# Kernel optimization log

Hardware: AMD Instinct MI355X
Metric: run time of the kernel (lower is better)

The kernel has to match this reference:

```python
import jax, jax.numpy as jnp
import numpy as np

DIM = 1024
NUM_HEADS = 16
HEAD_DIM = DIM // NUM_HEADS


def setup_inputs() -> dict:
    key = jax.random.key(0)
    k1, k2, k3, k4 = jax.random.split(key, 4)
    x = jax.random.normal(k1, (4, 4096, DIM), dtype=jnp.float32)
    # nn.Linear(dim, 3*dim, bias=False): weight [3*dim, dim]
    w_qkv = jax.random.normal(k2, (3 * DIM, DIM), dtype=jnp.float32) * (1.0 / np.sqrt(DIM))
    # nn.Linear(dim, dim): weight [dim, dim], bias [dim]
    w_proj = jax.random.normal(k3, (DIM, DIM), dtype=jnp.float32) * (1.0 / np.sqrt(DIM))
    b_proj = jax.random.normal(k4, (DIM,), dtype=jnp.float32) * 0.01
    return {"x": x, "w_qkv": w_qkv, "w_proj": w_proj, "b_proj": b_proj}


def reference(x, w_qkv, w_proj, b_proj):
    B, N, C = x.shape
    H, D = NUM_HEADS, C // NUM_HEADS
    # qkv projection: [B,N,3C] -> [3,B,H,N,D]
    qkv = (x @ w_qkv.T).reshape(B, N, 3, H, D).transpose(2, 0, 3, 1, 4)
    q, k, v = qkv[0], qkv[1], qkv[2]
    # elu(x)+1 feature map
    q = jax.nn.elu(q) + 1.0
    k = jax.nn.elu(k) + 1.0
    # kv outer-product aggregation: [B,H,D,D]
    kv = jnp.einsum('bhnd,bhne->bhde', k, v)
    # numerator: [B,H,N,D]
    num = jnp.einsum('bhnd,bhde->bhne', q, kv)
    # normalizer: [B,H,N]
    z = 1.0 / (jnp.einsum('bhnd,bhd->bhn', q, k.sum(axis=2)) + 1e-6)
    out = num * z[..., None]  # [B,H,N,D]
    out = out.transpose(0, 2, 1, 3).reshape(B, N, C)
    return out @ w_proj.T + b_proj
```

## Files before the change

kernel.cpp:

```cpp
#include <hip/hip_runtime.h>
#include <hip/hip_bf16.h>
#include <stdint.h>


typedef unsigned short u16;
typedef __attribute__((ext_vector_type(4))) float f32x4;
typedef __attribute__((ext_vector_type(8))) __bf16 bf16x8;
typedef __attribute__((ext_vector_type(4))) unsigned short us4;
typedef __attribute__((ext_vector_type(8))) unsigned short us8;

typedef __attribute__((address_space(3))) unsigned as3u;
typedef const __attribute__((address_space(1))) unsigned as1u;

__device__ __forceinline__ float bf2f(u16 u) {
  union { unsigned i; float f; } x; x.i = ((unsigned)u) << 16; return x.f;
}
__device__ __forceinline__ u16 f2bf(float f) {
  union { float f; unsigned i; } x; x.f = f;
  return (u16)((x.i + 0x7FFFu + ((x.i >> 16) & 1u)) >> 16);
}
__device__ __forceinline__ void gload16(const u16* g, u16* l) {
  __builtin_amdgcn_global_load_lds((as1u*)g, (as3u*)l, 16, 0, 0);
}
__device__ __forceinline__ bf16x8 ld8(const u16* p) { return *(const bf16x8*)p; }

#define BAR asm volatile("s_barrier" ::: "memory")
#define VMC4 asm volatile("s_waitcnt vmcnt(4)" ::: "memory")
#define VMC0 asm volatile("s_waitcnt vmcnt(0)" ::: "memory")

__global__ __launch_bounds__(256) void cvt_kernel(const float* __restrict__ src,
                                                  u16* __restrict__ dst, int n4) {
  int i = blockIdx.x * 256 + threadIdx.x;
  if (i < n4) {
    f32x4 v = ((const f32x4*)src)[i];
    us4 o;
    o[0] = f2bf(v[0]); o[1] = f2bf(v[1]); o[2] = f2bf(v[2]); o[3] = f2bf(v[3]);
    ((us4*)dst)[i] = o;
  }
}

template <int EPI>
__global__ __launch_bounds__(512) void gemm256(
    const u16* __restrict__ A, const u16* __restrict__ B, int Ncols,
    u16* __restrict__ oQ, u16* __restrict__ oKT, u16* __restrict__ oVT,
    const float* __restrict__ bias, float* __restrict__ oF) {
  constexpr int K = 1024;
  constexpr int NITER = 8;
  __shared__ u16 lds[2][2][256 * 64];

  const int nTn = Ncols >> 8;
  const int nwg = gridDim.x;
  const int bid = blockIdx.x;
  const int swz = (bid & 7) * (nwg >> 3) + (bid >> 3);
  const int tm = swz / nTn, tn = swz % nTn;
  const int m0 = tm << 8, n0 = tn << 8;
  const int t = threadIdx.x;
  const int w = t >> 6, lane = t & 63;
  const int wm = w >> 2, wn = w & 3;
  const int l15 = lane & 15, l4 = lane >> 4;

  const u16* Ab = A + (size_t)m0 * K;
  const u16* Bb = B + (size_t)n0 * K;

  int srcoff[2][2];
  #pragma unroll
  for (int l = 0; l < 2; ++l) {
    int c = l * 512 + t;
    int row = c >> 3, ch = c & 7;
    #pragma unroll
    for (int h = 0; h < 2; ++h) {
      int r = row + h * 128;
      srcoff[l][h] = r * K + (ch ^ (r & 7)) * 8;
    }
  }

#define STAGE(mat, buf, h, kt)                                                \
  {                                                                           \
    const u16* gsrc = ((mat) ? Bb : Ab) + (kt) * 64;                          \
    _Pragma("unroll") for (int l = 0; l < 2; ++l)                             \
        gload16(gsrc + srcoff[l][h],                                          \
                &lds[buf][mat][(l * 512 + w * 64) * 8 + (h) * 128 * 64]);     \
  }

#define LDA(buf, q)                                                           \
  _Pragma("unroll") for (int i = 0; i < 2; ++i)                               \
  _Pragma("unroll") for (int kk = 0; kk < 2; ++kk) {                          \
    int row = wm * 128 + (q) * 32 + i * 16 + l15;                             \
    int ch = (kk * 4 + l4) ^ (row & 7);                                       \
    a[i][kk] = ld8(&lds[buf][0][row * 64 + ch * 8]);                          \
  }

#define LDB(buf)                                                              \
  _Pragma("unroll") for (int j = 0; j < 4; ++j)                               \
  _Pragma("unroll") for (int kk = 0; kk < 2; ++kk) {                          \
    int row = wn * 64 + j * 16 + l15;                                         \
    int ch = (kk * 4 + l4) ^ (row & 7);                                       \
    b[j][kk] = ld8(&lds[buf][1][row * 64 + ch * 8]);                          \
  }

#define MFMA16(q)                                                             \
  __builtin_amdgcn_s_setprio(1);                                              \
  _Pragma("unroll") for (int i = 0; i < 2; ++i)                               \
  _Pragma("unroll") for (int kk = 0; kk < 2; ++kk)                            \
  _Pragma("unroll") for (int j = 0; j < 4; ++j)                               \
    acc[(q) * 2 + i][j] = __builtin_amdgcn_mfma_f32_16x16x32_bf16(            \
        a[i][kk], b[j][kk], acc[(q) * 2 + i][j], 0, 0, 0);                    \
  __builtin_amdgcn_s_setprio(0);

  f32x4 acc[8][4] = {};
  bf16x8 a[2][2], b[4][2];

  STAGE(1, 0, 0, 0); STAGE(1, 0, 1, 0);
  STAGE(0, 0, 0, 0); STAGE(0, 0, 1, 0);
  STAGE(1, 1, 0, 1); STAGE(1, 1, 1, 1);
  VMC4;
  BAR;

  for (int J = 0; J < NITER; ++J) {
    const int t2 = 2 * J + 2, t3 = 2 * J + 3;
    const bool more = (J < NITER - 1);
    LDB(0); LDA(0, 0);
    STAGE(0, 1, 0, 2 * J + 1);
    BAR; MFMA16(0); BAR;
    LDA(0, 1);
    STAGE(0, 1, 1, 2 * J + 1);
    BAR; MFMA16(1); BAR;
    LDA(0, 2);
    if (more) STAGE(1, 0, 0, t2);
    BAR; MFMA16(2); BAR;
    LDA(0, 3);
    if (more) STAGE(1, 0, 1, t2);
    BAR; MFMA16(3);
    if (more) { VMC4; } else { VMC0; }
    BAR;
    LDB(1); LDA(1, 0);
    if (more) STAGE(0, 0, 0, t2);
    BAR; MFMA16(0); BAR;
    LDA(1, 1);
    if (more) STAGE(0, 0, 1, t2);
    BAR; MFMA16(1); BAR;
    LDA(1, 2);
    if (more) STAGE(1, 1, 0, t3);
    BAR; MFMA16(2); BAR;
    LDA(1, 3);
    if (more) STAGE(1, 1, 1, t3);
    BAR; MFMA16(3);
    if (more) { VMC4; } else { VMC0; }
    BAR;
  }

  if constexpr (EPI == 0) {
    #pragma unroll
    for (int j = 0; j < 4; ++j) {
      const int col = n0 + wn * 64 + j * 16 + l15;
      const int part = col >> 10, cc = col & 1023;
      const int h = cc >> 6, d = cc & 63;
      #pragma unroll
      for (int fi = 0; fi < 8; ++fi) {
        const int mbase = m0 + wm * 128 + fi * 16 + l4 * 4;
        const int bb = mbase >> 12, n = mbase & 4095;
        const int bh = bb * 16 + h;
        if (part == 0) {
          #pragma unroll
          for (int r = 0; r < 4; ++r) {
            float val = acc[fi][j][r];
            val = val > 0.f ? val + 1.f : __expf(val);
            oQ[(((size_t)bh) * 4096 + n + r) * 64 + d] = f2bf(val);
          }
        } else {
          us4 o;
          #pragma unroll
          for (int r = 0; r < 4; ++r) {
            float val = acc[fi][j][r];
            if (part == 1) val = val > 0.f ? val + 1.f : __expf(val);
            o[r] = f2bf(val);
          }
          u16* dst = (part == 1) ? oKT : oVT;
          *(us4*)&dst[(((size_t)bh) * 64 + d) * 4096 + n] = o;
        }
      }
    }
  } else {
    #pragma unroll
    for (int fi = 0; fi < 8; ++fi) {
      const int mbase = m0 + wm * 128 + fi * 16 + l4 * 4;
      #pragma unroll
      for (int j = 0; j < 4; ++j) {
        const int col = n0 + wn * 64 + j * 16 + l15;
        #pragma unroll
        for (int r = 0; r < 4; ++r)
          oF[(size_t)(mbase + r) * 1024 + col] = acc[fi][j][r] + bias[col];
      }
    }
  }
#undef STAGE
#undef LDA
#undef LDB
#undef MFMA16
}

__global__ __launch_bounds__(256) void kv_mfma(const u16* __restrict__ kTg,
                                               const u16* __restrict__ vTg,
                                               float* __restrict__ kv_part,
                                               float* __restrict__ ksum_part) {
  __shared__ u16 kTl[64 * 256];
  __shared__ u16 vTl[64 * 256];
  const int blk = blockIdx.x;
  const int bh = blk >> 4, s = blk & 15;
  const int n0 = s * 256;
  const int t = threadIdx.x;
  const int w = t >> 6, lane = t & 63;
  const int wr = w >> 1, wc = w & 1;
  const int l15 = lane & 15, l4 = lane >> 4;

  const u16* kg = kTg + ((size_t)bh * 64) * 4096 + n0;
  const u16* vg = vTg + ((size_t)bh * 64) * 4096 + n0;
  #pragma unroll
  for (int i = 0; i < 8; ++i) {
    int c = i * 256 + t;
    int row = c >> 5, ch = c & 31;
    int sch = (ch & ~7) | ((ch ^ row) & 7);
    gload16(kg + (size_t)row * 4096 + sch * 8, &kTl[(i * 256 + w * 64) * 8]);
    gload16(vg + (size_t)row * 4096 + sch * 8, &vTl[(i * 256 + w * 64) * 8]);
  }
  __syncthreads();

  {
    const int row = t >> 2, q4 = t & 3;
    float sum = 0.f;
    #pragma unroll
    for (int j = 0; j < 8; ++j) {
      int p = q4 * 8 + ((j + row) & 7);
      us8 u = *(const us8*)&kTl[row * 256 + p * 8];
      #pragma unroll
      for (int x = 0; x < 8; ++x) sum += bf2f(u[x]);
    }
    sum += __shfl_xor(sum, 1);
    sum += __shfl_xor(sum, 2);
    if ((t & 3) == 0) ksum_part[((size_t)s * 64 + bh) * 64 + row] = sum;
  }

  f32x4 acc[2][2] = {};
  #pragma unroll
  for (int kk = 0; kk < 8; ++kk) {
    bf16x8 a[2], b[2];
    #pragma unroll
    for (int i = 0; i < 2; ++i) {
      int row = wr * 32 + i * 16 + l15;
      int p = (kk * 4 + l4) ^ (row & 7);
      a[i] = ld8(&kTl[row * 256 + p * 8]);
    }
    #pragma unroll
    for (int j = 0; j < 2; ++j) {
      int row = wc * 32 + j * 16 + l15;
      int p = (kk * 4 + l4) ^ (row & 7);
      b[j] = ld8(&vTl[row * 256 + p * 8]);
    }
    #pragma unroll
    for (int i = 0; i < 2; ++i)
      #pragma unroll
      for (int j = 0; j < 2; ++j)
        acc[i][j] = __builtin_amdgcn_mfma_f32_16x16x32_bf16(a[i], b[j], acc[i][j], 0, 0, 0);
  }
  float* dst = kv_part + ((size_t)s * 64 + bh) * 4096;
  #pragma unroll
  for (int i = 0; i < 2; ++i)
    #pragma unroll
    for (int j = 0; j < 2; ++j)
      #pragma unroll
      for (int r = 0; r < 4; ++r) {
        int d = wr * 32 + i * 16 + l4 * 4 + r;
        int e = wc * 32 + j * 16 + l15;
        dst[e * 64 + d] = acc[i][j][r];
      }
}

__global__ __launch_bounds__(256) void cvt_kv(const float* __restrict__ kv_part,
                                              const float* __restrict__ ksum_part,
                                              u16* __restrict__ kvTb) {
  const int bh = blockIdx.x;
  const int t = threadIdx.x;
  #pragma unroll
  for (int i = 0; i < 20; ++i) {
    int idx = i * 256 + t;
    int row = idx >> 6, d = idx & 63;
    float s = 0.f;
    if (row < 64) {
      #pragma unroll
      for (int p = 0; p < 16; ++p)
        s += kv_part[((size_t)p * 64 + bh) * 4096 + idx];
    } else if (row == 64) {
      #pragma unroll
      for (int p = 0; p < 16; ++p)
        s += ksum_part[((size_t)p * 64 + bh) * 64 + d];
    }
    kvTb[(size_t)bh * 5120 + idx] = f2bf(s);
  }
}

__global__ __launch_bounds__(256) void numz_mfma(const u16* __restrict__ qg,
                                                 const u16* __restrict__ kvTb,
                                                 u16* __restrict__ attn) {
  __shared__ u16 ql[128 * 64];
  __shared__ u16 bl[80 * 64];
  const int blk = blockIdx.x;
  const int bh = blk >> 5, c5 = blk & 31;
  const int t = threadIdx.x;
  const int w = t >> 6, lane = t & 63;
  const int l15 = lane & 15, l4 = lane >> 4;
  const int bb = bh >> 4, h = bh & 15;

  const u16* qp = qg + ((size_t)bh * 4096 + c5 * 128) * 64;
  #pragma unroll
  for (int i = 0; i < 4; ++i) {
    int c = i * 256 + t;
    int row = c >> 3, ch = c & 7;
    gload16(qp + (size_t)row * 64 + ((ch ^ row) & 7) * 8, &ql[(i * 256 + w * 64) * 8]);
  }
  {
    const us4* bsrc = (const us4*)(kvTb + (size_t)bh * 5120);
    #pragma unroll
    for (int i = 0; i < 5; ++i) {
      int idx = i * 256 + t;
      int row = idx >> 4;
      ((us4*)bl)[idx ^ ((row & 7) << 1)] = bsrc[idx];
    }
  }
  __syncthreads();

  f32x4 acc[2][5] = {};
  #pragma unroll
  for (int kk = 0; kk < 2; ++kk) {
    bf16x8 a[2], b[5];
    #pragma unroll
    for (int i = 0; i < 2; ++i) {
      int row = w * 32 + i * 16 + l15;
      int p = (kk * 4 + l4) ^ (row & 7);
      a[i] = ld8(&ql[row * 64 + p * 8]);
    }
    #pragma unroll
    for (int j = 0; j < 5; ++j) {
      int row = j * 16 + l15;
      int p = (kk * 4 + l4) ^ (row & 7);
      b[j] = ld8(&bl[row * 64 + p * 8]);
    }
    #pragma unroll
    for (int i = 0; i < 2; ++i)
      #pragma unroll
      for (int j = 0; j < 5; ++j)
        acc[i][j] = __builtin_amdgcn_mfma_f32_16x16x32_bf16(a[i], b[j], acc[i][j], 0, 0, 0);
  }

  #pragma unroll
  for (int i = 0; i < 2; ++i)
    #pragma unroll
    for (int r = 0; r < 4; ++r) {
      int m = w * 32 + i * 16 + l4 * 4 + r;
      int n = c5 * 128 + m;
      float zv = __shfl(acc[i][4][r], lane & 48);
      float zz = 1.f / (zv + 1e-6f);
      u16* op = attn + ((size_t)bb * 4096 + n) * 1024 + h * 64;
      #pragma unroll
      for (int j = 0; j < 4; ++j)
        op[j * 16 + l15] = f2bf(acc[i][j][r] * zz);
    }
}

extern "C" void kernel_launch(void* const* d_in, const int* in_sizes, int n_in,
                              void* d_out, int out_size, void* d_ws, size_t ws_size,
                              hipStream_t stream) {
  const float* x = (const float*)d_in[0];
  const float* w_qkv = (const float*)d_in[1];
  const float* w_proj = (const float*)d_in[2];
  const float* b_proj = (const float*)d_in[3];
  float* out = (float*)d_out;
  char* ws = (char*)d_ws;

  u16* xb        = (u16*)(ws);
  float* kv_part = (float*)(ws);
  u16* attn      = (u16*)(ws);
  u16* wqkvb     = (u16*)(ws + 33554432);
  u16* wprojb    = (u16*)(ws + 39845888);
  u16* q         = (u16*)(ws + 41943040);
  u16* kT        = (u16*)(ws + 75497472);
  u16* vT        = (u16*)(ws + 109051904);
  float* ksum_p  = (float*)(ws + 142606336);
  u16* kvTb      = (u16*)(ws + 142868480);

  cvt_kernel<<<16384, 256, 0, stream>>>(x, xb, 4194304);
  cvt_kernel<<<3072, 256, 0, stream>>>(w_qkv, wqkvb, 786432);
  cvt_kernel<<<1024, 256, 0, stream>>>(w_proj, wprojb, 262144);
  gemm256<0><<<64 * 12, 512, 0, stream>>>(xb, wqkvb, 3072, q, kT, vT, nullptr, nullptr);
  kv_mfma<<<1024, 256, 0, stream>>>(kT, vT, kv_part, ksum_p);
  cvt_kv<<<64, 256, 0, stream>>>(kv_part, ksum_p, kvTb);
  numz_mfma<<<2048, 256, 0, stream>>>(q, kvTb, attn);
  gemm256<1><<<64 * 4, 512, 0, stream>>>(attn, wprojb, 1024, nullptr, nullptr, nullptr,
                                         b_proj, out);
}
```

Baseline: 317.2 us.

## Stage Q epilogue through LDS for coalesced 16-byte stores; hardcode tile mapping

For the Q part of the QKV GEMM, the accumulators are written to LDS with an XOR swizzle and then read back as 8-element vectors, so each thread issues 16-byte coalesced global stores instead of scattered 2-byte ones. The block-to-tile mapping is also replaced with a fixed formula that assumes 64 M-tiles and groups blocks along M. This cuts store transactions for Q but adds two barriers and an LDS round trip. The hardcoded mapping only holds for this grid shape, and the GEMM instance with a different Ncols may also use it.

Result: faster. 309.5 us (-2.4%).

```diff
diff --git a/kernel.cpp b/kernel.cpp
--- a/kernel.cpp
+++ b/kernel.cpp
@@ -48,11 +48,9 @@
   constexpr int NITER = 8;
   __shared__ u16 lds[2][2][256 * 64];
 
-  const int nTn = Ncols >> 8;
-  const int nwg = gridDim.x;
   const int bid = blockIdx.x;
-  const int swz = (bid & 7) * (nwg >> 3) + (bid >> 3);
-  const int tm = swz / nTn, tn = swz % nTn;
+  const int tm = (bid & 7) * 8 + ((bid >> 3) & 7);
+  const int tn = bid >> 6;
   const int m0 = tm << 8, n0 = tn << 8;
   const int t = threadIdx.x;
   const int w = t >> 6, lane = t & 63;
@@ -150,24 +148,47 @@
   }
 
   if constexpr (EPI == 0) {
-    #pragma unroll
-    for (int j = 0; j < 4; ++j) {
-      const int col = n0 + wn * 64 + j * 16 + l15;
-      const int part = col >> 10, cc = col & 1023;
-      const int h = cc >> 6, d = cc & 63;
+    const int part = n0 >> 10;
+    if (part == 0) {
+      u16* sb = (u16*)lds;
+      __syncthreads();
       #pragma unroll
       for (int fi = 0; fi < 8; ++fi) {
-        const int mbase = m0 + wm * 128 + fi * 16 + l4 * 4;
-        const int bb = mbase >> 12, n = mbase & 4095;
-        const int bh = bb * 16 + h;
-        if (part == 0) {
+        #pragma unroll
+        for (int j = 0; j < 4; ++j) {
           #pragma unroll
           for (int r = 0; r < 4; ++r) {
+            int m = wm * 128 + fi * 16 + l4 * 4 + r;
+            int c = wn * 64 + j * 16 + l15;
             float val = acc[fi][j][r];
             val = val > 0.f ? val + 1.f : __expf(val);
-            oQ[(((size_t)bh) * 4096 + n + r) * 64 + d] = f2bf(val);
+            sb[m * 256 + (c ^ (((m >> 2) & 3) << 4))] = f2bf(val);
           }
-        } else {
+        }
+      }
+      __syncthreads();
+      #pragma unroll
+      for (int i = 0; i < 16; ++i) {
+        int idx = i * 512 + t;
+        int rr = idx >> 5, g = idx & 31;
+        int gs = g ^ (((rr >> 2) & 3) << 1);
+        us8 vv = *(const us8*)&sb[rr * 256 + gs * 8];
+        int n = (m0 + rr) & 4095, bb = (m0 + rr) >> 12;
+        int c = n0 + g * 8;
+        int h = c >> 6, d = c & 63;
+        *(us8*)&oQ[(((size_t)(bb * 16 + h)) * 4096 + n) * 64 + d] = vv;
+      }
+    } else {
+      #pragma unroll
+      for (int j = 0; j < 4; ++j) {
+        const int col = n0 + wn * 64 + j * 16 + l15;
+        const int cc = col & 1023;
+        const int h = cc >> 6, d = cc & 63;
+        #pragma unroll
+        for (int fi = 0; fi < 8; ++fi) {
+          const int mbase = m0 + wm * 128 + fi * 16 + l4 * 4;
+          const int bb = mbase >> 12, n = mbase & 4095;
+          const int bh = bb * 16 + h;
           us4 o;
           #pragma unroll
           for (int r = 0; r < 4; ++r) {
```
